# Optimization experiments

Measured on AMD Instinct MI355X. Metric: run time of the kernel, lower is better.

Reference implementation:

```python
import jax, jax.numpy as jnp
import numpy as np

VOCAB, EMB, HID, NTAG, SEQ = 50000, 256, 512, 20, 8192
H = HID // 2  # per-direction hidden size


def _lstm_dir(x, Wih, Whh, bih, bhh, reverse):
    # x: [S, E]; PyTorch gate order i, f, g, o
    h0 = jnp.zeros((H,), x.dtype)
    c0 = jnp.zeros((H,), x.dtype)
    b = bih + bhh
    xg = x @ Wih.T + b  # [S, 4H] precompute input projection

    def step(carry, xt):
        h, c = carry
        gates = xt + h @ Whh.T
        i, f, g, o = jnp.split(gates, 4)
        i = jax.nn.sigmoid(i)
        f = jax.nn.sigmoid(f)
        g = jnp.tanh(g)
        o = jax.nn.sigmoid(o)
        c = f * c + i * g
        h = o * jnp.tanh(c)
        return (h, c), h

    _, hs = jax.lax.scan(step, (h0, c0), xg, reverse=reverse)
    return hs  # [S, H]


def _viterbi(emissions, start_trans, end_trans, trans):
    # emissions [S, T]; torchcrf-style Viterbi decode
    score0 = start_trans + emissions[0]

    def fwd(score, em):
        tot = score[:, None] + trans          # [T_from, T_to]
        bp = jnp.argmax(tot, axis=0)          # best previous tag per next tag
        score = jnp.max(tot, axis=0) + em
        return score, bp

    final, bps = jax.lax.scan(fwd, score0, emissions[1:])
    final = final + end_trans
    last = jnp.argmax(final).astype(jnp.int32)

    def back(tag, bp):
        prev = bp[tag].astype(jnp.int32)
        return prev, prev

    _, prevs = jax.lax.scan(back, last, bps, reverse=True)
    return jnp.concatenate([prevs, last[None]])  # [S]


def setup_inputs() -> dict:
    key = jax.random.key(0)
    ks = jax.random.split(key, 16)
    s = 0.1
    inp = {
        "sentence": jax.random.randint(ks[0], (SEQ,), 0, VOCAB, dtype=jnp.int64)
                    if jax.config.read("jax_enable_x64") else
                    jax.random.randint(ks[0], (SEQ,), 0, VOCAB, dtype=jnp.int32),
        "embed": jax.random.normal(ks[1], (VOCAB, EMB), jnp.float32),
        "Wih_f": jax.random.normal(ks[2], (4 * H, EMB), jnp.float32) * s,
        "Whh_f": jax.random.normal(ks[3], (4 * H, H), jnp.float32) * s,
        "bih_f": jax.random.normal(ks[4], (4 * H,), jnp.float32) * s,
        "bhh_f": jax.random.normal(ks[5], (4 * H,), jnp.float32) * s,
        "Wih_b": jax.random.normal(ks[6], (4 * H, EMB), jnp.float32) * s,
        "Whh_b": jax.random.normal(ks[7], (4 * H, H), jnp.float32) * s,
        "bih_b": jax.random.normal(ks[8], (4 * H,), jnp.float32) * s,
        "bhh_b": jax.random.normal(ks[9], (4 * H,), jnp.float32) * s,
        "Wout": jax.random.normal(ks[10], (NTAG, HID), jnp.float32) * s,
        "bout": jax.random.normal(ks[11], (NTAG,), jnp.float32) * s,
        "start_trans": jax.random.normal(ks[12], (NTAG,), jnp.float32) * s,
        "end_trans": jax.random.normal(ks[13], (NTAG,), jnp.float32) * s,
        "trans": jax.random.normal(ks[14], (NTAG, NTAG), jnp.float32) * s,
    }
    return inp


def reference(sentence, embed, Wih_f, Whh_f, bih_f, bhh_f,
              Wih_b, Whh_b, bih_b, bhh_b, Wout, bout,
              start_trans, end_trans, trans):
    x = embed[sentence]                                  # [S, E]
    h_f = _lstm_dir(x, Wih_f, Whh_f, bih_f, bhh_f, reverse=False)
    h_b = _lstm_dir(x, Wih_b, Whh_b, bih_b, bhh_b, reverse=True)
    lstm_out = jnp.concatenate([h_f, h_b], axis=-1)      # [S, HID]; dropout is eval-mode identity
    emissions = lstm_out @ Wout.T + bout                 # [S, T]
    path = _viterbi(emissions, start_trans, end_trans, trans)
    return path
```

## Files before the change

kernel.cpp:

```cpp
#include <hip/hip_runtime.h>
#include <hip/hip_bf16.h>


#define S    8192
#define E    256
#define Hh   256
#define G    1024
#define NT   20
#define NB   4
#define NCHUNK 128
#define CLEN   64
#define SENT 0x7FC0DEADu

__global__ __launch_bounds__(256) void sentinel_fill(unsigned int* __restrict__ lo_u)
{
    size_t base = (size_t)blockIdx.x * 1024 + threadIdx.x;
    #pragma unroll
    for (int i = 0; i < 4; ++i)
        __hip_atomic_store(&lo_u[base + (size_t)i * 256], SENT,
                           __ATOMIC_RELAXED, __HIP_MEMORY_SCOPE_AGENT);
}

__global__ __launch_bounds__(512, 2) void xg_project(
    const int* __restrict__ sent, const float* __restrict__ embed,
    const float* __restrict__ Wih_f, const float* __restrict__ bih_f, const float* __restrict__ bhh_f,
    const float* __restrict__ Wih_b, const float* __restrict__ bih_b, const float* __restrict__ bhh_b,
    float* __restrict__ xg)
{
    const int tb  = blockIdx.x;
    const int rb  = blockIdx.y;
    const int dir = blockIdx.z;
    const int tid  = threadIdx.x;
    const int half = tid >> 8;
    const int idx  = tid & 255;
    const int r    = rb * 256 + idx;
    const float* Wih = dir ? Wih_b : Wih_f;

    __shared__ __align__(16) float4 xs4[32 * 64];
    __shared__ float psum[512];

    const int t0 = tb * 32;
    #pragma unroll
    for (int i = 0; i < 4; ++i) {
        int q   = i * 512 + tid;
        int row = q >> 6;
        int c4  = q & 63;
        int widx = sent[t0 + row];
        xs4[q] = *(const float4*)(embed + (size_t)widx * E + (size_t)c4 * 4);
    }

    float w[128];
    #pragma unroll
    for (int k = 0; k < 128; k += 4) {
        float4 v = *(const float4*)(Wih + (size_t)r * E + half * 128 + k);
        w[k] = v.x; w[k+1] = v.y; w[k+2] = v.z; w[k+3] = v.w;
    }
    float bias = 0.f;
    if (tid < 256) bias = dir ? (bih_b[r] + bhh_b[r]) : (bih_f[r] + bhh_f[r]);
    __syncthreads();

    const float* xs = (const float*)xs4 + half * 128;
    float* outb = xg + ((size_t)dir * S + t0) * G + r;
    for (int tt = 0; tt < 32; ++tt) {
        float a0 = 0.f, a1 = 0.f, a2 = 0.f, a3 = 0.f;
        #pragma unroll
        for (int k = 0; k < 128; k += 4) {
            float4 h4 = *(const float4*)(xs + tt * E + k);
            a0 = fmaf(w[k],   h4.x, a0);
            a1 = fmaf(w[k+1], h4.y, a1);
            a2 = fmaf(w[k+2], h4.z, a2);
            a3 = fmaf(w[k+3], h4.w, a3);
        }
        psum[tid] = (a0 + a1) + (a2 + a3);
        __syncthreads();
        if (tid < 256)
            outb[(size_t)tt * G] = bias + (psum[tid] + psum[tid + 256]);
        __syncthreads();
    }
}

__global__ __launch_bounds__(512, 2) void lstm_scan_mc(
    const float* __restrict__ xg,
    const float* __restrict__ Whh_f,
    const float* __restrict__ Whh_b,
    float* __restrict__ out)
{
    const int b    = blockIdx.x;
    const int dir  = blockIdx.y;
    const int tid  = threadIdx.x;
    const int half = tid >> 8;
    const int idx  = tid & 255;
    const int gate = idx >> 6;
    const int hloc = idx & 63;
    const int hidx = b * 64 + hloc;
    const int row  = gate * Hh + hidx;
    const float* W   = dir ? Whh_b : Whh_f;
    const float* xgd = xg + (size_t)dir * S * G;

    float w[128];
    #pragma unroll
    for (int k = 0; k < 128; k += 4) {
        float4 v = *(const float4*)(W + (size_t)row * Hh + half * 128 + k);
        w[k] = v.x; w[k+1] = v.y; w[k+2] = v.z; w[k+3] = v.w;
    }

    __shared__ __align__(16) float h_lds[Hh];
    __shared__ float psum[512];
    __shared__ float gates_lds[256];
    if (tid < Hh) h_lds[tid] = 0.f;
    float c = 0.f;

    const int t0 = dir ? (S - 1) : 0;
    const int dt = dir ? -1 : 1;
    float xg_cur = (tid < 256) ? xgd[(size_t)t0 * G + row] : 0.f;
    __syncthreads();

    for (int s = 0; s < S; ++s) {
        const int t = t0 + dt * s;
        float xg_next = 0.f;
        if (tid < 256 && s + 1 < S) xg_next = xgd[(size_t)(t + dt) * G + row];

        const float* hh = h_lds + half * 128;
        float a0 = 0.f, a1 = 0.f, a2 = 0.f, a3 = 0.f;
        #pragma unroll
        for (int k = 0; k < 128; k += 4) {
            float4 h4 = *(const float4*)(hh + k);
            a0 = fmaf(w[k],   h4.x, a0);
            a1 = fmaf(w[k+1], h4.y, a1);
            a2 = fmaf(w[k+2], h4.z, a2);
            a3 = fmaf(w[k+3], h4.w, a3);
        }
        psum[tid] = (a0 + a1) + (a2 + a3);
        __syncthreads();

        if (tid < 256) {
            float acc = xg_cur + (psum[idx] + psum[idx + 256]);
            float a = (gate == 2) ? tanhf(acc) : 1.f / (1.f + expf(-acc));
            gates_lds[idx] = a;
        }
        __syncthreads();

        if (tid < 64) {
            float iv = gates_lds[hloc];
            float fv = gates_lds[64 + hloc];
            float gv = gates_lds[128 + hloc];
            float ov = gates_lds[192 + hloc];
            c = fv * c + iv * gv;
            float h = ov * tanhf(c);
            __hip_atomic_store(out + (size_t)t * 512 + dir * Hh + hidx, h,
                               __ATOMIC_RELAXED, __HIP_MEMORY_SCOPE_AGENT);
            h_lds[hidx] = h;
        }
        if (s + 1 < S && tid < Hh && (tid >> 6) != b) {
            const unsigned int* srcp =
                (const unsigned int*)(out + (size_t)t * 512 + dir * Hh + tid);
            unsigned int v;
            do {
                v = __hip_atomic_load(srcp, __ATOMIC_RELAXED,
                                      __HIP_MEMORY_SCOPE_AGENT);
            } while (v == SENT);
            h_lds[tid] = __uint_as_float(v);
        }
        __syncthreads();
        xg_cur = xg_next;
    }
}

__global__ __launch_bounds__(256) void emissions_kernel(
    const float* __restrict__ lo,
    const float* __restrict__ Wout,
    const float* __restrict__ bout,
    float* __restrict__ em)
{
    int gid = blockIdx.x * blockDim.x + threadIdx.x;
    if (gid >= S * NT) return;
    int t = gid / NT;
    int j = gid - t * NT;
    const float* x = lo + (size_t)t * 512;
    const float* w = Wout + (size_t)j * 512;
    float a0 = 0.f, a1 = 0.f, a2 = 0.f, a3 = 0.f;
    #pragma unroll 8
    for (int k = 0; k < 512; k += 4) {
        float4 xv = *(const float4*)(x + k);
        float4 wv = *(const float4*)(w + k);
        a0 = fmaf(xv.x, wv.x, a0);
        a1 = fmaf(xv.y, wv.y, a1);
        a2 = fmaf(xv.z, wv.z, a2);
        a3 = fmaf(xv.w, wv.w, a3);
    }
    em[gid] = bout[j] + ((a0 + a1) + (a2 + a3));
}

__global__ __launch_bounds__(64) void viterbi_fwd(
    const float* __restrict__ em,
    const float* __restrict__ start_trans,
    const float* __restrict__ end_trans,
    const float* __restrict__ trans,
    unsigned char* __restrict__ bp,
    int* __restrict__ last_out)
{
    const int j = threadIdx.x;
    const bool act = (j < NT);
    __shared__ __align__(16) float sc[2][NT];

    float tc[NT];
    if (act) {
        #pragma unroll
        for (int i = 0; i < NT; ++i) tc[i] = trans[i * NT + j];
        sc[0][j] = start_trans[j] + em[j];
        bp[j] = (unsigned char)j;
    }
    __syncthreads();

    float e_cur = act ? em[NT + j] : 0.f;
    for (int t = 1; t < S; ++t) {
        float e_nxt = (act && t + 1 < S) ? em[(size_t)(t + 1) * NT + j] : 0.f;

        const float* sp = sc[(t - 1) & 1];
        float s0[NT];
        #pragma unroll
        for (int i = 0; i < NT; i += 4) {
            float4 v = *(const float4*)(sp + i);
            s0[i] = v.x; s0[i+1] = v.y; s0[i+2] = v.z; s0[i+3] = v.w;
        }
        float bestv = s0[0] + tc[0];
        int   besti = 0;
        #pragma unroll
        for (int i = 1; i < NT; ++i) {
            float v = s0[i] + tc[i];
            if (v > bestv) { bestv = v; besti = i; }
        }
        if (act) {
            sc[t & 1][j] = bestv + e_cur;
            bp[(size_t)t * NT + j] = (unsigned char)besti;
        }
        __syncthreads();
        e_cur = e_nxt;
    }

    if (j == 0) {
        const float* sp = sc[(S - 1) & 1];
        float bv = sp[0] + end_trans[0];
        int   bi = 0;
        for (int i = 1; i < NT; ++i) {
            float v = sp[i] + end_trans[i];
            if (v > bv) { bv = v; bi = i; }
        }
        *last_out = bi;
    }
}

__global__ __launch_bounds__(64) void bt_maps(
    const unsigned char* __restrict__ bp, unsigned char* __restrict__ maps)
{
    __shared__ unsigned char lbp[CLEN * NT];
    const int c = blockIdx.x, tid = threadIdx.x;
    const unsigned* src = (const unsigned*)(bp + (size_t)c * CLEN * NT);
    unsigned* dst = (unsigned*)lbp;
    for (int q = tid; q < CLEN * NT / 4; q += 64) dst[q] = src[q];
    __syncthreads();
    if (tid < NT) {
        int x = tid;
        for (int t = CLEN - 1; t >= 0; --t) x = lbp[t * NT + x];
        maps[c * NT + tid] = (unsigned char)x;
    }
}

__global__ __launch_bounds__(64) void bt_boundary(
    const unsigned char* __restrict__ maps, const int* __restrict__ last_out,
    int* __restrict__ btags)
{
    __shared__ unsigned char m[NCHUNK * NT];
    const int tid = threadIdx.x;
    for (int q = tid; q < NCHUNK * NT; q += 64) m[q] = maps[q];
    __syncthreads();
    if (tid == 0) {
        int x = *last_out;
        btags[NCHUNK - 1] = x;
        for (int c = NCHUNK - 1; c >= 1; --c) {
            x = m[c * NT + x];
            btags[c - 1] = x;
        }
    }
}

__global__ __launch_bounds__(64) void bt_emit(
    const unsigned char* __restrict__ bp, const int* __restrict__ btags,
    int* __restrict__ path)
{
    __shared__ unsigned char lbp[CLEN * NT];
    const int c = blockIdx.x, tid = threadIdx.x;
    const unsigned* src = (const unsigned*)(bp + (size_t)c * CLEN * NT);
    unsigned* dst = (unsigned*)lbp;
    for (int q = tid; q < CLEN * NT / 4; q += 64) dst[q] = src[q];
    __syncthreads();
    if (tid == 0) {
        int x = btags[c];
        path[c * CLEN + CLEN - 1] = x;
        for (int t = CLEN - 1; t >= 1; --t) {
            x = lbp[t * NT + x];
            path[c * CLEN + t - 1] = x;
        }
    }
}

extern "C" void kernel_launch(void* const* d_in, const int* in_sizes, int n_in,
                              void* d_out, int out_size, void* d_ws, size_t ws_size,
                              hipStream_t stream) {
    const int*   sent   = (const int*)  d_in[0];
    const float* embed  = (const float*)d_in[1];
    const float* Wih_f  = (const float*)d_in[2];
    const float* Whh_f  = (const float*)d_in[3];
    const float* bih_f  = (const float*)d_in[4];
    const float* bhh_f  = (const float*)d_in[5];
    const float* Wih_b  = (const float*)d_in[6];
    const float* Whh_b  = (const float*)d_in[7];
    const float* bih_b  = (const float*)d_in[8];
    const float* bhh_b  = (const float*)d_in[9];
    const float* Wout   = (const float*)d_in[10];
    const float* bout   = (const float*)d_in[11];
    const float* start_trans = (const float*)d_in[12];
    const float* end_trans   = (const float*)d_in[13];
    const float* trans       = (const float*)d_in[14];
    int* path = (int*)d_out;

    char* ws = (char*)d_ws;
    size_t off = 0;
    float* xg = (float*)(ws + off); off += (size_t)2 * S * G * 4;
    float* lo = (float*)(ws + off); off += (size_t)S * 512 * 4;
    float* em = (float*)(ws + off); off += (size_t)S * NT * 4;
    unsigned char* bp   = (unsigned char*)(ws + off); off += (size_t)S * NT;
    unsigned char* maps = (unsigned char*)(ws + off); off += 4096;
    int* btags = (int*)(ws + off); off += 1024;
    int* lastp = (int*)(ws + off); off += 256;

    sentinel_fill<<<dim3(4096), 256, 0, stream>>>((unsigned int*)lo);
    xg_project<<<dim3(S / 32, 4, 2), 512, 0, stream>>>(
        sent, embed, Wih_f, bih_f, bhh_f, Wih_b, bih_b, bhh_b, xg);
    lstm_scan_mc<<<dim3(NB, 2), 512, 0, stream>>>(xg, Whh_f, Whh_b, lo);
    emissions_kernel<<<dim3((S * NT + 255) / 256), 256, 0, stream>>>(lo, Wout, bout, em);
    viterbi_fwd<<<dim3(1), 64, 0, stream>>>(em, start_trans, end_trans, trans, bp, lastp);
    bt_maps<<<dim3(NCHUNK), 64, 0, stream>>>(bp, maps);
    bt_boundary<<<dim3(1), 64, 0, stream>>>(maps, lastp, btags);
    bt_emit<<<dim3(NCHUNK), 64, 0, stream>>>(bp, btags, path);
}
```

Before: 17.87 ms.

## Split LSTM and projection dot products four ways; shuffle-based Viterbi forward

Raises xg_project and lstm_scan_mc to 1024-thread blocks so each gate row's dot product is split across four 64-element slices instead of two 128-element halves. This halves per-thread register weights and serial FMA chain length on the sequential recurrence, at the cost of a four-way LDS reduction and more threads at each barrier. Viterbi forward is rewritten to spread the 20x20 max over 60 lanes (3 groups of 7 sources) using wavefront shuffles, removing shared memory and the per-step __syncthreads.

```diff
diff --git a/kernel.cpp b/kernel.cpp
--- a/kernel.cpp
+++ b/kernel.cpp
@@ -21,7 +21,7 @@
                            __ATOMIC_RELAXED, __HIP_MEMORY_SCOPE_AGENT);
 }
 
-__global__ __launch_bounds__(512, 2) void xg_project(
+__global__ __launch_bounds__(1024, 4) void xg_project(
     const int* __restrict__ sent, const float* __restrict__ embed,
     const float* __restrict__ Wih_f, const float* __restrict__ bih_f, const float* __restrict__ bhh_f,
     const float* __restrict__ Wih_b, const float* __restrict__ bih_b, const float* __restrict__ bhh_b,
@@ -30,41 +30,41 @@
     const int tb  = blockIdx.x;
     const int rb  = blockIdx.y;
     const int dir = blockIdx.z;
-    const int tid  = threadIdx.x;
-    const int half = tid >> 8;
-    const int idx  = tid & 255;
-    const int r    = rb * 256 + idx;
+    const int tid = threadIdx.x;
+    const int q   = tid >> 8;
+    const int idx = tid & 255;
+    const int r   = rb * 256 + idx;
     const float* Wih = dir ? Wih_b : Wih_f;
 
     __shared__ __align__(16) float4 xs4[32 * 64];
-    __shared__ float psum[512];
+    __shared__ float psum[1024];
 
     const int t0 = tb * 32;
     #pragma unroll
-    for (int i = 0; i < 4; ++i) {
-        int q   = i * 512 + tid;
-        int row = q >> 6;
-        int c4  = q & 63;
+    for (int i = 0; i < 2; ++i) {
+        int qq  = i * 1024 + tid;
+        int row = qq >> 6;
+        int c4  = qq & 63;
         int widx = sent[t0 + row];
-        xs4[q] = *(const float4*)(embed + (size_t)widx * E + (size_t)c4 * 4);
-    }
-
-    float w[128];
-    #pragma unroll
-    for (int k = 0; k < 128; k += 4) {
-        float4 v = *(const float4*)(Wih + (size_t)r * E + half * 128 + k);
+        xs4[qq] = *(const float4*)(embed + (size_t)widx * E + (size_t)c4 * 4);
+    }
+
+    float w[64];
+    #pragma unroll
+    for (int k = 0; k < 64; k += 4) {
+        float4 v = *(const float4*)(Wih + (size_t)r * E + q * 64 + k);
         w[k] = v.x; w[k+1] = v.y; w[k+2] = v.z; w[k+3] = v.w;
     }
     float bias = 0.f;
     if (tid < 256) bias = dir ? (bih_b[r] + bhh_b[r]) : (bih_f[r] + bhh_f[r]);
     __syncthreads();
 
-    const float* xs = (const float*)xs4 + half * 128;
+    const float* xs = (const float*)xs4 + q * 64;
     float* outb = xg + ((size_t)dir * S + t0) * G + r;
     for (int tt = 0; tt < 32; ++tt) {
         float a0 = 0.f, a1 = 0.f, a2 = 0.f, a3 = 0.f;
         #pragma unroll
-        for (int k = 0; k < 128; k += 4) {
+        for (int k = 0; k < 64; k += 4) {
             float4 h4 = *(const float4*)(xs + tt * E + k);
             a0 = fmaf(w[k],   h4.x, a0);
             a1 = fmaf(w[k+1], h4.y, a1);
@@ -74,12 +74,13 @@
         psum[tid] = (a0 + a1) + (a2 + a3);
         __syncthreads();
         if (tid < 256)
-            outb[(size_t)tt * G] = bias + (psum[tid] + psum[tid + 256]);
-        __syncthreads();
-    }
-}
-
-__global__ __launch_bounds__(512, 2) void lstm_scan_mc(
+            outb[(size_t)tt * G] = bias +
+                ((psum[idx] + psum[idx + 256]) + (psum[idx + 512] + psum[idx + 768]));
+        __syncthreads();
+    }
+}
+
+__global__ __launch_bounds__(1024, 4) void lstm_scan_mc(
     const float* __restrict__ xg,
     const float* __restrict__ Whh_f,
     const float* __restrict__ Whh_b,
@@ -88,7 +89,7 @@
     const int b    = blockIdx.x;
     const int dir  = blockIdx.y;
     const int tid  = threadIdx.x;
-    const int half = tid >> 8;
+    const int q    = tid >> 8;
     const int idx  = tid & 255;
     const int gate = idx >> 6;
     const int hloc = idx & 63;
@@ -97,15 +98,15 @@
     const float* W   = dir ? Whh_b : Whh_f;
     const float* xgd = xg + (size_t)dir * S * G;
 
-    float w[128];
-    #pragma unroll
-    for (int k = 0; k < 128; k += 4) {
-        float4 v = *(const float4*)(W + (size_t)row * Hh + half * 128 + k);
+    float w[64];
+    #pragma unroll
+    for (int k = 0; k < 64; k += 4) {
+        float4 v = *(const float4*)(W + (size_t)row * Hh + q * 64 + k);
         w[k] = v.x; w[k+1] = v.y; w[k+2] = v.z; w[k+3] = v.w;
     }
 
     __shared__ __align__(16) float h_lds[Hh];
-    __shared__ float psum[512];
+    __shared__ float psum[1024];
     __shared__ float gates_lds[256];
     if (tid < Hh) h_lds[tid] = 0.f;
     float c = 0.f;
@@ -120,10 +121,10 @@
         float xg_next = 0.f;
         if (tid < 256 && s + 1 < S) xg_next = xgd[(size_t)(t + dt) * G + row];
 
-        const float* hh = h_lds + half * 128;
+        const float* hh = (const float*)h_lds + q * 64;
         float a0 = 0.f, a1 = 0.f, a2 = 0.f, a3 = 0.f;
         #pragma unroll
-        for (int k = 0; k < 128; k += 4) {
+        for (int k = 0; k < 64; k += 4) {
             float4 h4 = *(const float4*)(hh + k);
             a0 = fmaf(w[k],   h4.x, a0);
             a1 = fmaf(w[k+1], h4.y, a1);
@@ -134,7 +135,8 @@
         __syncthreads();
 
         if (tid < 256) {
-            float acc = xg_cur + (psum[idx] + psum[idx + 256]);
+            float acc = xg_cur +
+                ((psum[idx] + psum[idx + 256]) + (psum[idx + 512] + psum[idx + 768]));
             float a = (gate == 2) ? tanhf(acc) : 1.f / (1.f + expf(-acc));
             gates_lds[idx] = a;
         }
@@ -199,55 +201,55 @@
     unsigned char* __restrict__ bp,
     int* __restrict__ last_out)
 {
-    const int j = threadIdx.x;
-    const bool act = (j < NT);
-    __shared__ __align__(16) float sc[2][NT];
-
-    float tc[NT];
-    if (act) {
+    const int lane = threadIdx.x;
+    const int g    = lane / 20;
+    const int j    = lane - g * 20;
+    const int i0   = g * 7;
+
+    float tc[7];
+    #pragma unroll
+    for (int u = 0; u < 7; ++u) {
+        int i = i0 + u;
+        tc[u] = (g < 3 && i < 20) ? trans[i * NT + j] : -3.0e38f;
+    }
+
+    const int jj = (g < 3) ? j : 0;
+    float snew  = start_trans[jj] + em[jj];
+    if (g == 0) bp[j] = (unsigned char)j;
+    float e_cur = em[NT + jj];
+
+    for (int t = 1; t < S; ++t) {
+        float s_sub[7];
         #pragma unroll
-        for (int i = 0; i < NT; ++i) tc[i] = trans[i * NT + j];
-        sc[0][j] = start_trans[j] + em[j];
-        bp[j] = (unsigned char)j;
-    }
-    __syncthreads();
-
-    float e_cur = act ? em[NT + j] : 0.f;
-    for (int t = 1; t < S; ++t) {
-        float e_nxt = (act && t + 1 < S) ? em[(size_t)(t + 1) * NT + j] : 0.f;
-
-        const float* sp = sc[(t - 1) & 1];
-        float s0[NT];
+        for (int u = 0; u < 7; ++u)
+            s_sub[u] = __shfl(snew, i0 + u);
+        float e_nxt = (t + 1 < S) ? em[(size_t)(t + 1) * NT + jj] : 0.f;
+
+        float bv = s_sub[0] + tc[0];
+        int   bi = i0;
         #pragma unroll
-        for (int i = 0; i < NT; i += 4) {
-            float4 v = *(const float4*)(sp + i);
-            s0[i] = v.x; s0[i+1] = v.y; s0[i+2] = v.z; s0[i+3] = v.w;
-        }
-        float bestv = s0[0] + tc[0];
-        int   besti = 0;
-        #pragma unroll
-        for (int i = 1; i < NT; ++i) {
-            float v = s0[i] + tc[i];
-            if (v > bestv) { bestv = v; besti = i; }
-        }
-        if (act) {
-            sc[t & 1][j] = bestv + e_cur;
-            bp[(size_t)t * NT + j] = (unsigned char)besti;
-        }
-        __syncthreads();
+        for (int u = 1; u < 7; ++u) {
+            float v = s_sub[u] + tc[u];
+            if (v > bv) { bv = v; bi = i0 + u; }
+        }
+        float v0 = __shfl(bv, jj), v1 = __shfl(bv, jj + 20), v2 = __shfl(bv, jj + 40);
+        int   c0 = __shfl(bi, jj), c1 = __shfl(bi, jj + 20), c2 = __shfl(bi, jj + 40);
+        float best = v0; int bidx = c0;
+        if (v1 > best) { best = v1; bidx = c1; }
+        if (v2 > best) { best = v2; bidx = c2; }
+        snew = best + e_cur;
+        if (g == 0) bp[(size_t)t * NT + j] = (unsigned char)bidx;
         e_cur = e_nxt;
     }
 
-    if (j == 0) {
-        const float* sp = sc[(S - 1) & 1];
-        float bv = sp[0] + end_trans[0];
-        int   bi = 0;
-        for (int i = 1; i < NT; ++i) {
-            float v = sp[i] + end_trans[i];
-            if (v > bv) { bv = v; bi = i; }
-        }
-        *last_out = bi;
-    }
+    float bv = __shfl(snew, 0) + end_trans[0];
+    int   bi = 0;
+    #pragma unroll 1
+    for (int i = 1; i < 20; ++i) {
+        float v = __shfl(snew, i) + end_trans[i];
+        if (v > bv) { bv = v; bi = i; }
+    }
+    if (lane == 0) *last_out = bi;
 }
 
 __global__ __launch_bounds__(64) void bt_maps(
@@ -335,9 +337,9 @@
     int* lastp = (int*)(ws + off); off += 256;
 
     sentinel_fill<<<dim3(4096), 256, 0, stream>>>((unsigned int*)lo);
-    xg_project<<<dim3(S / 32, 4, 2), 512, 0, stream>>>(
+    xg_project<<<dim3(S / 32, 4, 2), 1024, 0, stream>>>(
         sent, embed, Wih_f, bih_f, bhh_f, Wih_b, bih_b, bhh_b, xg);
-    lstm_scan_mc<<<dim3(NB, 2), 512, 0, stream>>>(xg, Whh_f, Whh_b, lo);
+    lstm_scan_mc<<<dim3(NB, 2), 1024, 0, stream>>>(xg, Whh_f, Whh_b, lo);
     emissions_kernel<<<dim3((S * NT + 255) / 256), 256, 0, stream>>>(lo, Wout, bout, em);
     viterbi_fwd<<<dim3(1), 64, 0, stream>>>(em, start_trans, end_trans, trans, bp, lastp);
     bt_maps<<<dim3(NCHUNK), 64, 0, stream>>>(bp, maps);
```

New measurement: 15.61 ms. 1.14x faster.
